# Optimization experiments

Measured on AMD Instinct MI355X. Metric: run time of the kernel, lower is better.

Reference implementation:

```python
import jax, jax.numpy as jnp
import numpy as np

DIM = 2048            # model dim
HID = 4096            # ssm inner dim (multiple_of*round(2/3*6144))
H = 64                # n_heads
P = HID // H          # head_dim = 64
N = 128               # state_dim
G = 1                 # n_groups
K = 4                 # conv_size
Q = 128               # chunk_size
CONV_DIM = HID + 2 * G * N       # 4352
D_IN = 2 * HID + 2 * G * N + H   # 8512
EPS = 1e-5


def _causal_conv_silu(xBC, w):
    # xBC: [B,L,C], w: [C,K]; depthwise causal conv1d fused with SiLU
    kern = w.T[:, None, :]  # [K,1,C]
    y = jax.lax.conv_general_dilated(
        xBC, kern, window_strides=(1,), padding=[(K - 1, 0)],
        dimension_numbers=('NHC', 'HIO', 'NHC'),
        feature_group_count=xBC.shape[-1])
    return y * jax.nn.sigmoid(y)


def _ssm(x, W_in, conv_w, dt_bias, A_log, D, norm_w, W_out):
    Bsz, L, _ = x.shape
    zxbcdt = x @ W_in.T                       # [B,L,D_IN]
    z = zxbcdt[..., :HID]                     # gate
    xBC = zxbcdt[..., HID:HID + CONV_DIM]
    dt_raw = zxbcdt[..., HID + CONV_DIM:]     # [B,L,H]

    xBC = _causal_conv_silu(xBC, conv_w)
    xs = xBC[..., :HID].reshape(Bsz, L, H, P)
    rep = H // G
    Bh = jnp.repeat(xBC[..., HID:HID + G * N].reshape(Bsz, L, G, N), rep, axis=2)  # [B,L,H,N]
    Ch = jnp.repeat(xBC[..., HID + G * N:].reshape(Bsz, L, G, N), rep, axis=2)

    dt = jax.nn.softplus(dt_raw + dt_bias)    # [B,L,H], dt_softplus=True
    A = -jnp.exp(A_log)                       # [H]

    # ---- chunked selective scan (Mamba2 SSD), chunk size Q ----
    nc = L // Q
    a = (dt * A).reshape(Bsz, nc, Q, H)
    cum = jnp.cumsum(a, axis=2)               # inclusive within-chunk cumsum, <= 0
    xs_c = xs.reshape(Bsz, nc, Q, H, P)
    dtc = dt.reshape(Bsz, nc, Q, H)
    Bc = Bh.reshape(Bsz, nc, Q, H, N)
    Cc = Ch.reshape(Bsz, nc, Q, H, N)

    # intra-chunk (diagonal) part: Y[i] += sum_{j<=i} exp(cum_i-cum_j) dt_j (C_i.B_j) x_j
    diff = cum[:, :, :, None, :] - cum[:, :, None, :, :]     # [b,c,i,j,h]
    tril = jnp.tril(jnp.ones((Q, Q), bool))[None, None, :, :, None]
    Lmat = jnp.exp(jnp.where(tril, diff, -jnp.inf))          # causal decay matrix
    CB = jnp.einsum('bcihn,bcjhn->bcijh', Cc, Bc)
    M = CB * Lmat * dtc[:, :, None, :, :]
    Yd = jnp.einsum('bcijh,bcjhp->bcihp', M, xs_c)

    # per-chunk end state: sum_j exp(cum_last-cum_j) dt_j x_j (x) B_j
    wdec = jnp.exp(cum[:, :, -1:, :] - cum) * dtc            # [b,c,q,h]
    states = jnp.einsum('bcqh,bcqhn,bcqhp->bchpn', wdec, Bc, xs_c)
    chunk_decay = jnp.exp(cum[:, :, -1, :])                  # [b,c,h]

    # inter-chunk recurrence over nc chunks
    def step(S, inp):
        dec, st = inp                                        # [b,h], [b,h,p,n]
        return S * dec[..., None, None] + st, S              # emit state entering chunk
    S0 = jnp.zeros((Bsz, H, P, N), x.dtype)
    _, Sprev = jax.lax.scan(step, S0,
                            (chunk_decay.transpose(1, 0, 2),
                             states.transpose(1, 0, 2, 3, 4)))
    Sprev = Sprev.transpose(1, 0, 2, 3, 4)                   # [b,c,h,p,n]

    # inter-chunk (off-diagonal) contribution
    Yoff = jnp.einsum('bcqh,bcqhn,bchpn->bcqhp', jnp.exp(cum), Cc, Sprev)

    y = (Yd + Yoff).reshape(Bsz, L, H, P) + D[None, None, :, None] * xs  # skip D
    y = y.reshape(Bsz, L, HID)

    yz = y * (z * jax.nn.sigmoid(z))                         # gated: y * silu(z)
    yn = yz * jax.lax.rsqrt(jnp.mean(yz * yz, axis=-1, keepdims=True) + EPS) * norm_w
    return yn @ W_out.T


def setup_inputs() -> dict:
    key = jax.random.key(0)
    k = jax.random.split(key, 6)
    return {
        'x': jax.random.normal(k[0], (2, 4096, DIM), jnp.float32),
        'W_in': jax.random.normal(k[1], (D_IN, DIM), jnp.float32) * DIM ** -0.5,
        'conv_w': jax.random.normal(k[2], (CONV_DIM, K), jnp.float32) * K ** -0.5,
        'dt_bias': jax.random.uniform(k[3], (H,), jnp.float32, minval=0.001, maxval=0.1),
        'A_log': jnp.log(jax.random.uniform(k[4], (H,), jnp.float32, minval=1.0, maxval=16.0)),
        'D': jnp.ones((H,), jnp.float32),
        'norm_w': jnp.ones((HID,), jnp.float32),
        'W_out': jax.random.normal(k[5], (DIM, HID), jnp.float32) * HID ** -0.5,
    }


def reference(x, W_in, conv_w, dt_bias, A_log, D, norm_w, W_out):
    return _ssm(x, W_in, conv_w, dt_bias, A_log, D, norm_w, W_out)
```

## Files before the change

### kernel.cpp

```cpp
#include <hip/hip_runtime.h>
#include <hip/hip_fp16.h>
#include <math.h>

#define ROWS   8192
#define DIMK   2048
#define HIDN   4096
#define QCH    128
#define NCHUNK 32

typedef __attribute__((ext_vector_type(8))) short short8;
typedef __attribute__((ext_vector_type(8))) _Float16 half8;
typedef __attribute__((ext_vector_type(4))) float floatx4;

static __device__ inline unsigned short f2h(float f){
  union { _Float16 h; unsigned short u; } v; v.h = (_Float16)f; return v.u;
}
static __device__ inline float h2f(unsigned short u){
  union { unsigned short u; _Float16 h; } v; v.u = u; return (float)v.h;
}
static __device__ inline void async_cp16(const void* g, void* l){
  __builtin_amdgcn_global_load_lds((const __attribute__((address_space(1))) void*)g,
                                   (__attribute__((address_space(3))) void*)l, 16, 0, 0);
}

__global__ void k_cast(const float* __restrict__ in, unsigned short* __restrict__ out, int n4){
  int i = blockIdx.x * 256 + threadIdx.x;
  if (i < n4){
    float4 v = ((const float4*)in)[i];
    unsigned long long p = (unsigned long long)f2h(v.x)
                         | ((unsigned long long)f2h(v.y) << 16)
                         | ((unsigned long long)f2h(v.z) << 32)
                         | ((unsigned long long)f2h(v.w) << 48);
    ((unsigned long long*)out)[i] = p;
  }
}

__global__ __launch_bounds__(256)
void k_dtraw(const float* __restrict__ x, const float* __restrict__ Win,
             float* __restrict__ dtraw){
  __shared__ float ws[64 * 132];
  const int t = threadIdx.x;
  const int lane = t & 63, w = t >> 6;
  const int r0 = blockIdx.x * 16;
  const int rw = __builtin_amdgcn_readfirstlane(r0 + w * 4);
  float a0 = 0.f, a1 = 0.f, a2 = 0.f, a3 = 0.f;
  for (int k0 = 0; k0 < DIMK; k0 += 128){
    __syncthreads();
#pragma unroll
    for (int l = 0; l < 8; l++){
      int fidx = (l * 256 + t) * 4;
      int row = fidx >> 7, col = fidx & 127;
      *(float4*)&ws[row * 132 + col] =
          *(const float4*)&Win[(size_t)(8448 + row) * DIMK + k0 + col];
    }
    __syncthreads();
    const float* xp = x + (size_t)rw * DIMK + k0;
#pragma unroll 8
    for (int kk = 0; kk < 128; kk += 4){
      float4 wv = *(const float4*)&ws[lane * 132 + kk];
      float4 v0 = *(const float4*)&xp[kk];
      float4 v1 = *(const float4*)&xp[DIMK + kk];
      float4 v2 = *(const float4*)&xp[2*DIMK + kk];
      float4 v3 = *(const float4*)&xp[3*DIMK + kk];
      a0 += wv.x*v0.x + wv.y*v0.y + wv.z*v0.z + wv.w*v0.w;
      a1 += wv.x*v1.x + wv.y*v1.y + wv.z*v1.z + wv.w*v1.w;
      a2 += wv.x*v2.x + wv.y*v2.y + wv.z*v2.z + wv.w*v2.w;
      a3 += wv.x*v3.x + wv.y*v3.y + wv.z*v3.z + wv.w*v3.w;
    }
  }
  dtraw[(size_t)rw * 64 + lane]       = a0;
  dtraw[((size_t)rw + 1) * 64 + lane] = a1;
  dtraw[((size_t)rw + 2) * 64 + lane] = a2;
  dtraw[((size_t)rw + 3) * 64 + lane] = a3;
}

template<int KD>
__device__ inline void gemm256_core(const unsigned short* __restrict__ A,
                                    const unsigned short* __restrict__ B,
                                    int row0, int col0,
                                    unsigned short* sA, unsigned short* sB,
                                    floatx4 (&acc)[8][4], int t){
  const int lane = t & 63, wid = t >> 6;
  const int wm = wid >> 2, wn = wid & 3;
  const int quad = lane >> 4, l16 = lane & 15;
  const int srow  = t >> 3;
  const int sslot = (t & 7) ^ (srow & 7);
  constexpr int NT = KD / 64;

  auto stageA = [&](int d, int half, int kt){
    unsigned short* dst = sA + d*256*64 + half*128*64;
    const unsigned short* src = A + (size_t)(row0 + half*128) * KD + kt*64;
#pragma unroll
    for (int i = 0; i < 2; i++)
      async_cp16(src + (size_t)(i*64 + srow) * KD + sslot*8,
                 dst + ((size_t)i*512 + t)*8);
  };
  auto stageB = [&](int d, int half, int kt){
    unsigned short* dst = sB + d*256*64 + half*128*64;
    const unsigned short* src = B + (size_t)(col0 + half*128) * KD + kt*64;
#pragma unroll
    for (int i = 0; i < 2; i++)
      async_cp16(src + (size_t)(i*64 + srow) * KD + sslot*8,
                 dst + ((size_t)i*512 + t)*8);
  };

  half8 af[4][2], bf[2][2];
  auto loadA = [&](const unsigned short* cA, int h){
#pragma unroll
    for (int mm = 0; mm < 4; mm++)
#pragma unroll
      for (int ks = 0; ks < 2; ks++)
        af[mm][ks] = *(const half8*)&cA[((h*4+mm)*16 + l16)*64 + (((ks*4+quad)^(l16&7))*8)];
  };
  auto loadB = [&](const unsigned short* cB, int h){
#pragma unroll
    for (int nn = 0; nn < 2; nn++)
#pragma unroll
      for (int ks = 0; ks < 2; ks++)
        bf[nn][ks] = *(const half8*)&cB[((h*2+nn)*16 + l16)*64 + (((ks*4+quad)^(l16&7))*8)];
  };
  auto mmac = [&](int mh, int nh){
    __builtin_amdgcn_s_setprio(1);
#pragma unroll
    for (int mm = 0; mm < 4; mm++)
#pragma unroll
      for (int nn = 0; nn < 2; nn++)
#pragma unroll
        for (int ks = 0; ks < 2; ks++)
          acc[mh*4+mm][nh*2+nn] = __builtin_amdgcn_mfma_f32_16x16x32_f16(
              af[mm][ks], bf[nn][ks], acc[mh*4+mm][nh*2+nn], 0, 0, 0);
    __builtin_amdgcn_s_setprio(0);
  };

  stageA(0,0,0); stageA(0,1,0); stageB(0,0,0); stageB(0,1,0);
  stageA(1,0,1); stageA(1,1,1);
  asm volatile("s_waitcnt vmcnt(4)" ::: "memory");
  __builtin_amdgcn_s_barrier();

  for (int T = 0; T < NT; T++){
    const int cur = T & 1;
    const unsigned short* cA = sA + cur*256*64 + wm*128*64;
    const unsigned short* cB = sB + cur*256*64 + wn*64*64;
    loadA(cA, 0); loadB(cB, 0);
    if (T + 1 < NT) stageB(cur^1, 0, T+1);
    __builtin_amdgcn_s_barrier();
    mmac(0, 0);
    __builtin_amdgcn_s_barrier();
    loadB(cB, 1);
    if (T + 1 < NT) stageB(cur^1, 1, T+1);
    __builtin_amdgcn_s_barrier();
    mmac(0, 1);
    __builtin_amdgcn_s_barrier();
    loadA(cA, 1);
    if (T + 2 < NT) stageA(cur, 0, T+2);
    __builtin_amdgcn_s_barrier();
    mmac(1, 1);
    __builtin_amdgcn_s_barrier();
    loadB(cB, 0);
    if (T + 2 < NT) stageA(cur, 1, T+2);
    if (T + 2 < NT)      { asm volatile("s_waitcnt vmcnt(4)" ::: "memory"); }
    else if (T + 1 < NT) { asm volatile("s_waitcnt vmcnt(0)" ::: "memory"); }
    __builtin_amdgcn_s_barrier();
    mmac(1, 0);
    __builtin_amdgcn_s_barrier();
  }
}

__global__ __launch_bounds__(512, 2)
void k_gemm1(const unsigned short* __restrict__ A, const unsigned short* __restrict__ B,
             unsigned short* __restrict__ zbuf, unsigned short* __restrict__ xsraw,
             unsigned short* __restrict__ bcraw){
  __shared__ __align__(16) unsigned short sA[2*256*64];
  __shared__ __align__(16) unsigned short sB[2*256*64];
  const int t = threadIdx.x;
  int swz = (blockIdx.x % 8) * 132 + blockIdx.x / 8;
  const int row0 = (swz & 31) * 256, col0 = (swz >> 5) * 256;
  floatx4 acc[8][4] = {};
  gemm256_core<DIMK>(A, B, row0, col0, sA, sB, acc, t);
  const int lane = t & 63, wid = t >> 6;
  const int wm = wid >> 2, wn = wid & 3;
  const int quad = lane >> 4, l16 = lane & 15;
  unsigned short* dst; int cbase, ldd;
  if (col0 < 4096){ dst = zbuf; cbase = 0; ldd = 4096; }
  else if (col0 < 8192){ dst = xsraw; cbase = 4096; ldd = 4096; }
  else { dst = bcraw; cbase = 8192; ldd = 256; }
#pragma unroll
  for (int m = 0; m < 8; m++)
#pragma unroll
    for (int n = 0; n < 4; n++){
      int rb = row0 + wm*128 + m*16 + quad*4;
      int cc = col0 + wn*64 + n*16 + l16 - cbase;
#pragma unroll
      for (int r = 0; r < 4; r++)
        dst[(size_t)(rb + r) * ldd + cc] = f2h(acc[m][n][r]);
    }
}

__global__ __launch_bounds__(512, 2)
void k_gemm2(const unsigned short* __restrict__ A, const unsigned short* __restrict__ B,
             float* __restrict__ C){
  __shared__ __align__(16) unsigned short sA[2*256*64];
  __shared__ __align__(16) unsigned short sB[2*256*64];
  const int t = threadIdx.x;
  int swz = (blockIdx.x % 8) * 32 + blockIdx.x / 8;
  const int row0 = (swz & 31) * 256, col0 = (swz >> 5) * 256;
  floatx4 acc[8][4] = {};
  gemm256_core<HIDN>(A, B, row0, col0, sA, sB, acc, t);
  const int lane = t & 63, wid = t >> 6;
  const int wm = wid >> 2, wn = wid & 3;
  const int quad = lane >> 4, l16 = lane & 15;
#pragma unroll
  for (int m = 0; m < 8; m++)
#pragma unroll
    for (int n = 0; n < 4; n++){
      int rb = row0 + wm*128 + m*16 + quad*4;
      int cc = col0 + wn*64 + n*16 + l16;
#pragma unroll
      for (int r = 0; r < 4; r++)
        C[(size_t)(rb + r) * DIMK + cc] = acc[m][n][r];
    }
}

__global__ void k_halo(const unsigned short* __restrict__ xsraw, unsigned short* __restrict__ halo){
  int col = blockIdx.x * 256 + threadIdx.x;
  int slot = blockIdx.y, bc = blockIdx.z;
  long r = (long)bc * QCH - 3 + slot;
  if (r >= 0)
    halo[((size_t)bc * 3 + slot) * 4096 + col] = xsraw[(size_t)r * 4096 + col];
}

__global__ void k_convbc(const unsigned short* __restrict__ bcraw, const float* __restrict__ cw,
                         unsigned short* __restrict__ bcc){
  int row = blockIdx.x, c = threadIdx.x;
  int tl = row & 4095;
  const float4 wv = *(const float4*)&cw[(size_t)(4096 + c) * 4];
  const unsigned short* col = bcraw + c;
  size_t rb = (size_t)row * 256;
  float a = h2f(col[rb]) * wv.w;
  if (tl >= 1) a += h2f(col[rb - 256]) * wv.z;
  if (tl >= 2) a += h2f(col[rb - 512]) * wv.y;
  if (tl >= 3) a += h2f(col[rb - 768]) * wv.x;
  bcc[rb + c] = f2h(a / (1.f + __expf(-a)));
}

__global__ void k_dtcum(const float* __restrict__ dtraw, const float* __restrict__ dtbias,
                        const float* __restrict__ Alog, float* __restrict__ dtb,
                        float* __restrict__ cumb){
  int bc = blockIdx.x;
  int h  = threadIdx.x;
  float bias = dtbias[h];
  float A = -__expf(Alog[h]);
  float run = 0.f;
  size_t rowb = (size_t)bc * QCH;
  for (int q = 0; q < QCH; q++){
    float dr = dtraw[(rowb + q) * 64 + h] + bias;
    float dt = dr > 20.f ? dr : log1pf(__expf(dr));
    dtb[(rowb + q) * 64 + h] = dt;
    run += dt * A;
    cumb[(rowb + q) * 64 + h] = run;
  }
}

__device__ inline void stage_xsT(const unsigned short* __restrict__ xsraw,
                                 const unsigned short* __restrict__ halo,
                                 const float* cws, unsigned short* xsT,
                                 int bc, int h, int t){
  const size_t rowb = (size_t)bc * QCH;
  const int tl0 = (bc & 31) * QCH;
#pragma unroll
  for (int it = 0; it < 2; it++){
    int idx = it * 256 + t;
    int q = idx & 127, p0 = (idx >> 7) * 16;
    int tl = tl0 + q;
    const unsigned short* cur = xsraw + (rowb + q) * 4096 + h * 64 + p0;
    const unsigned short* hb  = halo + ((size_t)bc * 3) * 4096 + h * 64 + p0;
    const unsigned short* r1 = (q >= 1) ? cur - 4096     : hb + 2 * 4096;
    const unsigned short* r2 = (q >= 2) ? cur - 2 * 4096 : hb + (size_t)(q + 1) * 4096;
    const unsigned short* r3 = (q >= 3) ? cur - 3 * 4096 : hb + (size_t)q * 4096;
    float f1 = (tl >= 1) ? 1.f : 0.f;
    float f2 = (tl >= 2) ? 1.f : 0.f;
    float f3 = (tl >= 3) ? 1.f : 0.f;
    short8 c0 = *(const short8*)cur, c1 = *(const short8*)(cur + 8);
    short8 a0 = *(const short8*)r1,  a1 = *(const short8*)(r1 + 8);
    short8 b0 = *(const short8*)r2,  b1 = *(const short8*)(r2 + 8);
    short8 d0 = *(const short8*)r3,  d1 = *(const short8*)(r3 + 8);
#pragma unroll
    for (int j = 0; j < 16; j++){
      int col = p0 + j;
      const float* wp = cws + col * 4;
      float vc = h2f((unsigned short)(j < 8 ? c0[j] : c1[j-8]));
      float v1 = h2f((unsigned short)(j < 8 ? a0[j] : a1[j-8]));
      float v2 = h2f((unsigned short)(j < 8 ? b0[j] : b1[j-8]));
      float v3 = h2f((unsigned short)(j < 8 ? d0[j] : d1[j-8]));
      float a = vc * wp[3] + f1 * v1 * wp[2] + f2 * v2 * wp[1] + f3 * v3 * wp[0];
      float s = a / (1.f + __expf(-a));
      xsT[col * 128 + q] = f2h(s);
    }
  }
}

__global__ __launch_bounds__(256, 2)
void k_chunk1(const unsigned short* __restrict__ xsc, const unsigned short* __restrict__ bcc,
              const float* __restrict__ dtb, const float* __restrict__ cumb,
              const float* __restrict__ Dp, const unsigned short* __restrict__ st,
              unsigned short* __restrict__ ybuf){
  __shared__ __align__(16) unsigned short Ml[128*128];
  __shared__ __align__(16) unsigned short xsT[64*128];
  __shared__ float cum_s[128], dt_s[128];
  const int blk = blockIdx.x, h = blk & 63, bc = blk >> 6;
  const size_t rowb = (size_t)bc * QCH;
  const int t = threadIdx.x, w = t >> 6, lane = t & 63, quad = lane >> 4, l16 = lane & 15;
  const int wrow = w * 32;
  if (t < 128){ cum_s[t] = cumb[(rowb + t)*64 + h]; dt_s[t] = dtb[(rowb + t)*64 + h]; }
  __syncthreads();
#pragma unroll
  for (int it = 0; it < 2; it++){
    int idx = it * 256 + t;
    int q = idx & 127, p0 = (idx >> 7) * 16;
    const unsigned short* cur = xsc + (rowb + q) * 4096 + h * 64 + p0;
    short8 c0 = *(const short8*)cur, c1 = *(const short8*)(cur + 8);
#pragma unroll
    for (int j = 0; j < 16; j++)
      xsT[(p0 + j) * 128 + q] = (unsigned short)(j < 8 ? c0[j] : c1[j-8]);
  }
  floatx4 acc[2][8] = {};
  const unsigned short* Cb = bcc + rowb * 256 + 128;
  const unsigned short* Bb = bcc + rowb * 256;
#pragma unroll
  for (int ks = 0; ks < 4; ks++){
    half8 af[2];
#pragma unroll
    for (int i = 0; i < 2; i++)
      af[i] = *(const half8*)(Cb + (size_t)(wrow + i*16 + l16) * 256 + ks*32 + quad*8);
#pragma unroll
    for (int j = 0; j < 8; j++){
      half8 bfr = *(const half8*)(Bb + (size_t)(j*16 + l16) * 256 + ks*32 + quad*8);
#pragma unroll
      for (int i = 0; i < 2; i++)
        acc[i][j] = __builtin_amdgcn_mfma_f32_16x16x32_f16(af[i], bfr, acc[i][j], 0, 0, 0);
    }
  }
#pragma unroll
  for (int i = 0; i < 2; i++)
#pragma unroll
    for (int j = 0; j < 8; j++){
      int jc = j*16 + l16;
      float dtj = dt_s[jc], cj = cum_s[jc];
#pragma unroll
      for (int r = 0; r < 4; r++){
        int ir = wrow + i*16 + quad*4 + r;
        float m = (ir >= jc) ? acc[i][j][r] * __expf(cum_s[ir] - cj) * dtj : 0.f;
        Ml[ir * 128 + jc] = f2h(m);
      }
    }
  __syncthreads();
  floatx4 accY[2][4] = {};
#pragma unroll
  for (int ks = 0; ks < 4; ks++){
    half8 af[2], bfr[4];
#pragma unroll
    for (int i = 0; i < 2; i++)
      af[i] = *(const half8*)&Ml[(wrow + i*16 + l16)*128 + ks*32 + quad*8];
#pragma unroll
    for (int p = 0; p < 4; p++)
      bfr[p] = *(const half8*)&xsT[(p*16 + l16)*128 + ks*32 + quad*8];
#pragma unroll
    for (int i = 0; i < 2; i++)
#pragma unroll
      for (int p = 0; p < 4; p++)
        accY[i][p] = __builtin_amdgcn_mfma_f32_16x16x32_f16(af[i], bfr[p], accY[i][p], 0, 0, 0);
  }
  __syncthreads();
  unsigned short* Sp = Ml;
  {
    size_t base = ((size_t)bc * 64 + h) * 8192;
#pragma unroll
    for (int it = 0; it < 4; it++){
      int idx = (it * 256 + t) * 8;
      *(short8*)&Sp[idx] = *(const short8*)&st[base + idx];
    }
  }
  __syncthreads();
  floatx4 accO[2][4] = {};
#pragma unroll
  for (int ks = 0; ks < 4; ks++){
    half8 af[2], bfr[4];
#pragma unroll
    for (int i = 0; i < 2; i++)
      af[i] = *(const half8*)(Cb + (size_t)(wrow + i*16 + l16) * 256 + ks*32 + quad*8);
#pragma unroll
    for (int p = 0; p < 4; p++)
      bfr[p] = *(const half8*)&Sp[(p*16 + l16)*128 + ks*32 + quad*8];
#pragma unroll
    for (int i = 0; i < 2; i++)
#pragma unroll
      for (int p = 0; p < 4; p++)
        accO[i][p] = __builtin_amdgcn_mfma_f32_16x16x32_f16(af[i], bfr[p], accO[i][p], 0, 0, 0);
  }
  float Dh = Dp[h];
#pragma unroll
  for (int i = 0; i < 2; i++)
#pragma unroll
    for (int p = 0; p < 4; p++){
      int pc = p*16 + l16;
#pragma unroll
      for (int r = 0; r < 4; r++){
        int ir = wrow + i*16 + quad*4 + r;
        float y = accY[i][p][r] + __expf(cum_s[ir]) * accO[i][p][r] + Dh * h2f(xsT[pc*128 + ir]);
        ybuf[(rowb + ir) * (size_t)HIDN + h*64 + pc] = f2h(y);
      }
    }
}

__global__ __launch_bounds__(256, 2)
void k_chunk2(unsigned short* __restrict__ xsraw, const unsigned short* __restrict__ bcc,
              const unsigned short* __restrict__ halo, const float* __restrict__ cw,
              const float* __restrict__ dtb, const float* __restrict__ cumb,
              unsigned short* __restrict__ st){
  __shared__ __align__(16) unsigned short wBT[128*128];
  __shared__ __align__(16) unsigned short xsT[64*128];
  __shared__ float cum_s[128], dt_s[128];
  __shared__ float cws[64*4];
  const int blk = blockIdx.x, h = blk & 63, bc = blk >> 6;
  const size_t rowb = (size_t)bc * QCH;
  const int t = threadIdx.x, w = t >> 6, lane = t & 63, quad = lane >> 4, l16 = lane & 15;
  if (t < 128){ cum_s[t] = cumb[(rowb + t)*64 + h]; dt_s[t] = dtb[(rowb + t)*64 + h]; }
  if (t < 64) *(float4*)&cws[t*4] = *(const float4*)&cw[((size_t)h*64 + t)*4];
  __syncthreads();
  stage_xsT(xsraw, halo, cws, xsT, bc, h, t);
  __syncthreads();
#pragma unroll
  for (int it = 0; it < 2; it++){
    int idx = it * 256 + t;
    int q = idx & 127, p0 = (idx >> 7) * 16;
    short8 w0, w1;
#pragma unroll
    for (int j = 0; j < 8; j++){
      w0[j] = (short)xsT[(p0 + j) * 128 + q];
      w1[j] = (short)xsT[(p0 + 8 + j) * 128 + q];
    }
    unsigned short* g = xsraw + (rowb + q) * 4096 + h * 64 + p0;
    *(short8*)g = w0;
    *(short8*)(g + 8) = w1;
  }
  float clast = cum_s[127];
#pragma unroll
  for (int it = 0; it < 2; it++){
    int idx = it * 256 + t;
    int q = idx & 127, n0 = (idx >> 7) * 32;
    float wd = __expf(clast - cum_s[q]) * dt_s[q];
    const unsigned short* gp = bcc + (rowb + q) * 256 + n0;
#pragma unroll
    for (int c4 = 0; c4 < 4; c4++){
      short8 v = *(const short8*)(gp + c4*8);
#pragma unroll
      for (int jj = 0; jj < 8; jj++)
        wBT[(n0 + c4*8 + jj)*128 + q] = f2h(h2f((unsigned short)v[jj]) * wd);
    }
  }
  __syncthreads();
  floatx4 acc[8] = {};
#pragma unroll
  for (int ks = 0; ks < 4; ks++){
    half8 af = *(const half8*)&xsT[(w*16 + l16)*128 + ks*32 + quad*8];
#pragma unroll
    for (int j = 0; j < 8; j++){
      half8 bfr = *(const half8*)&wBT[(j*16 + l16)*128 + ks*32 + quad*8];
      acc[j] = __builtin_amdgcn_mfma_f32_16x16x32_f16(af, bfr, acc[j], 0, 0, 0);
    }
  }
  size_t base = ((size_t)bc * 64 + h) * 8192;
#pragma unroll
  for (int j = 0; j < 8; j++){
    int n = j*16 + l16;
#pragma unroll
    for (int r = 0; r < 4; r++){
      int p = w*16 + quad*4 + r;
      st[base + p*128 + n] = f2h(acc[j][r]);
    }
  }
}

__global__ void k_scan(unsigned short* __restrict__ st, const float* __restrict__ cumb){
  int id = blockIdx.x * 256 + threadIdx.x;
  int n = id & 127, p = (id >> 7) & 63, h = (id >> 13) & 63, b = id >> 19;
  float S = 0.f;
  for (int c = 0; c < NCHUNK; c++){
    int bc = b * NCHUNK + c;
    size_t idx = ((size_t)bc * 64 + h) * 8192 + (size_t)p * 128 + n;
    float dec = __expf(cumb[((size_t)bc * QCH + 127) * 64 + h]);
    float v = h2f(st[idx]);
    st[idx] = f2h(S);
    S = S * dec + v;
  }
}

__global__ __launch_bounds__(256)
void k_gate(unsigned short* __restrict__ yb, const unsigned short* __restrict__ zb,
            const float* __restrict__ nw){
  __shared__ float red[4];
  int row = blockIdx.x, t = threadIdx.x;
  float vals[16], ss = 0.f;
#pragma unroll
  for (int it = 0; it < 16; it++){
    int c = it * 256 + t;
    float y = h2f(yb[(size_t)row * HIDN + c]);
    float z = h2f(zb[(size_t)row * HIDN + c]);
    float v = y * (z / (1.f + __expf(-z)));
    vals[it] = v; ss += v * v;
  }
  for (int o = 32; o > 0; o >>= 1) ss += __shfl_down(ss, o, 64);
  int w = t >> 6, lane = t & 63;
  if (lane == 0) red[w] = ss;
  __syncthreads();
  float scale = rsqrtf((red[0] + red[1] + red[2] + red[3]) / (float)HIDN + 1e-5f);
#pragma unroll
  for (int it = 0; it < 16; it++){
    int c = it * 256 + t;
    yb[(size_t)row * HIDN + c] = f2h(vals[it] * scale * nw[c]);
  }
}

extern "C" void kernel_launch(void* const* d_in, const int* in_sizes, int n_in,
                              void* d_out, int out_size, void* d_ws, size_t ws_size,
                              hipStream_t stream){
  const float* x      = (const float*)d_in[0];
  const float* Win    = (const float*)d_in[1];
  const float* convw  = (const float*)d_in[2];
  const float* dtbias = (const float*)d_in[3];
  const float* Alog   = (const float*)d_in[4];
  const float* Dp     = (const float*)d_in[5];
  const float* nw     = (const float*)d_in[6];
  const float* Wout   = (const float*)d_in[7];
  float* out = (float*)d_out;

  char* ws = (char*)d_ws;
  size_t off = 0;
  auto alloc = [&](size_t bytes)->void*{ void* p = ws + off; off += (bytes + 255) & ~(size_t)255; return p; };
  unsigned short* xw    = (unsigned short*)alloc((size_t)ROWS * DIMK * 2);
  unsigned short* winb  = (unsigned short*)alloc((size_t)8448 * DIMK * 2);
  float*          dtraw = (float*)alloc((size_t)ROWS * 64 * 4);
  unsigned short* woutb = (unsigned short*)alloc((size_t)DIMK * HIDN * 2);
  unsigned short* zbuf  = (unsigned short*)alloc((size_t)ROWS * HIDN * 2);
  unsigned short* xsraw = (unsigned short*)alloc((size_t)ROWS * HIDN * 2);
  unsigned short* bcraw = (unsigned short*)alloc((size_t)ROWS * 256 * 2);
  unsigned short* bcc   = (unsigned short*)alloc((size_t)ROWS * 256 * 2);
  unsigned short* halo  = (unsigned short*)alloc((size_t)64 * 3 * 4096 * 2);
  float*          dtb   = (float*)alloc((size_t)ROWS * 64 * 4);
  float*          cumb  = (float*)alloc((size_t)ROWS * 64 * 4);
  unsigned short* st    = xw;
  unsigned short* ybuf  = xsraw;

  k_cast<<<(ROWS*DIMK/4 + 255)/256, 256, 0, stream>>>(x, xw, ROWS*DIMK/4);
  k_cast<<<(8448*DIMK/4 + 255)/256, 256, 0, stream>>>(Win, winb, 8448*DIMK/4);
  k_cast<<<(DIMK*HIDN/4 + 255)/256, 256, 0, stream>>>(Wout, woutb, DIMK*HIDN/4);
  k_dtraw<<<ROWS/16, 256, 0, stream>>>(x, Win, dtraw);
  k_gemm1<<<dim3(33*32), 512, 0, stream>>>(xw, winb, zbuf, xsraw, bcraw);
  k_halo<<<dim3(16, 3, 64), 256, 0, stream>>>(xsraw, halo);
  k_convbc<<<ROWS, 256, 0, stream>>>(bcraw, convw, bcc);
  k_dtcum<<<64, 64, 0, stream>>>(dtraw, dtbias, Alog, dtb, cumb);
  k_chunk2<<<4096, 256, 0, stream>>>(xsraw, bcc, halo, convw, dtb, cumb, st);
  k_scan<<<4096, 256, 0, stream>>>(st, cumb);
  k_chunk1<<<4096, 256, 0, stream>>>(xsraw, bcc, dtb, cumb, Dp, st, ybuf);
  k_gate<<<ROWS, 256, 0, stream>>>(ybuf, zbuf, nw);
  k_gemm2<<<dim3(8*32), 512, 0, stream>>>(ybuf, woutb, out);
}
```

Baseline: 1.197 ms.

## Hold full A/B fragment sets in registers with inline-asm LDS reads in GEMM core

The GEMM main loop now keeps all eight A fragments and four B fragments of the K-tile in registers instead of reloading halves. It issues explicit ds_read_b128 instructions behind sched_barrier and lgkmcnt waits, and reorders the MFMA quadrants so each fragment is read from LDS only once per tile. This cuts LDS read traffic and removes one barrier phase, and both A-tile prefetches now go out together. The cost is more VGPRs under launch_bounds(512,2), which risks spills, and the hard lgkmcnt(0) waits block the compiler from interleaving reads with MFMAs.

```diff
diff --git a/kernel.cpp b/kernel.cpp
--- a/kernel.cpp
+++ b/kernel.cpp
@@ -74,6 +74,18 @@
   dtraw[((size_t)rw + 3) * 64 + lane] = a3;
 }
 
+static __device__ inline unsigned ldsaddr(const void* p){
+  return (unsigned)(size_t)(const __attribute__((address_space(3))) void*)p;
+}
+static __device__ inline floatx4 dsr128(unsigned a){
+  floatx4 d;
+  asm volatile("ds_read_b128 %0, %1" : "=v"(d) : "v"(a));
+  return d;
+}
+static __device__ inline half8 as_h8(floatx4 f){
+  union { floatx4 f; half8 h; } u; u.f = f; return u.h;
+}
+
 template<int KD>
 __device__ inline void gemm256_core(const unsigned short* __restrict__ A,
                                     const unsigned short* __restrict__ B,
@@ -104,20 +116,13 @@
                  dst + ((size_t)i*512 + t)*8);
   };
 
-  half8 af[4][2], bf[2][2];
-  auto loadA = [&](const unsigned short* cA, int h){
-#pragma unroll
-    for (int mm = 0; mm < 4; mm++)
-#pragma unroll
-      for (int ks = 0; ks < 2; ks++)
-        af[mm][ks] = *(const half8*)&cA[((h*4+mm)*16 + l16)*64 + (((ks*4+quad)^(l16&7))*8)];
+  const unsigned sAbase = ldsaddr(sA), sBbase = ldsaddr(sB);
+  floatx4 af[8][2], bf[4][2];
+  auto rdA = [&](unsigned base, int fr, int ks) -> floatx4 {
+    return dsr128(base + 2u*(unsigned)((fr*16 + l16)*64 + (((ks*4+quad)^(l16&7))*8)));
   };
-  auto loadB = [&](const unsigned short* cB, int h){
-#pragma unroll
-    for (int nn = 0; nn < 2; nn++)
-#pragma unroll
-      for (int ks = 0; ks < 2; ks++)
-        bf[nn][ks] = *(const half8*)&cB[((h*2+nn)*16 + l16)*64 + (((ks*4+quad)^(l16&7))*8)];
+  auto rdB = [&](unsigned base, int fc, int ks) -> floatx4 {
+    return dsr128(base + 2u*(unsigned)((fc*16 + l16)*64 + (((ks*4+quad)^(l16&7))*8)));
   };
   auto mmac = [&](int mh, int nh){
     __builtin_amdgcn_s_setprio(1);
@@ -128,7 +133,7 @@
 #pragma unroll
         for (int ks = 0; ks < 2; ks++)
           acc[mh*4+mm][nh*2+nn] = __builtin_amdgcn_mfma_f32_16x16x32_f16(
-              af[mm][ks], bf[nn][ks], acc[mh*4+mm][nh*2+nn], 0, 0, 0);
+              as_h8(af[mh*4+mm][ks]), as_h8(bf[nh*2+nn][ks]), acc[mh*4+mm][nh*2+nn], 0, 0, 0);
     __builtin_amdgcn_s_setprio(0);
   };
 
@@ -139,29 +144,53 @@
 
   for (int T = 0; T < NT; T++){
     const int cur = T & 1;
-    const unsigned short* cA = sA + cur*256*64 + wm*128*64;
-    const unsigned short* cB = sB + cur*256*64 + wn*64*64;
-    loadA(cA, 0); loadB(cB, 0);
+    const unsigned aAd = sAbase + 2u*(unsigned)(cur*256*64 + wm*128*64);
+    const unsigned bAd = sBbase + 2u*(unsigned)(cur*256*64 + wn*64*64);
+#pragma unroll
+    for (int fr = 0; fr < 4; fr++)
+#pragma unroll
+      for (int ks = 0; ks < 2; ks++)
+        af[fr][ks] = rdA(aAd, fr, ks);
+#pragma unroll
+    for (int fc = 0; fc < 2; fc++)
+#pragma unroll
+      for (int ks = 0; ks < 2; ks++)
+        bf[fc][ks] = rdB(bAd, fc, ks);
     if (T + 1 < NT) stageB(cur^1, 0, T+1);
     __builtin_amdgcn_s_barrier();
+    asm volatile("s_waitcnt lgkmcnt(0)" ::: "memory");
+    __builtin_amdgcn_sched_barrier(0);
     mmac(0, 0);
     __builtin_amdgcn_s_barrier();
-    loadB(cB, 1);
+#pragma unroll
+    for (int fr = 4; fr < 8; fr++)
+#pragma unroll
+      for (int ks = 0; ks < 2; ks++)
+        af[fr][ks] = rdA(aAd, fr, ks);
     if (T + 1 < NT) stageB(cur^1, 1, T+1);
     __builtin_amdgcn_s_barrier();
+    asm volatile("s_waitcnt lgkmcnt(0)" ::: "memory");
+    __builtin_amdgcn_sched_barrier(0);
+    mmac(1, 0);
+    __builtin_amdgcn_s_barrier();
+#pragma unroll
+    for (int fc = 2; fc < 4; fc++)
+#pragma unroll
+      for (int ks = 0; ks < 2; ks++)
+        bf[fc][ks] = rdB(bAd, fc, ks);
+    __builtin_amdgcn_s_barrier();
+    asm volatile("s_waitcnt lgkmcnt(0)" ::: "memory");
+    __builtin_amdgcn_sched_barrier(0);
     mmac(0, 1);
     __builtin_amdgcn_s_barrier();
-    loadA(cA, 1);
-    if (T + 2 < NT) stageA(cur, 0, T+2);
+    if (T + 2 < NT){
+      stageA(cur, 0, T+2); stageA(cur, 1, T+2);
+      asm volatile("s_waitcnt vmcnt(4)" ::: "memory");
+    } else if (T + 1 < NT){
+      asm volatile("s_waitcnt vmcnt(0)" ::: "memory");
+    }
     __builtin_amdgcn_s_barrier();
     mmac(1, 1);
-    __builtin_amdgcn_s_barrier();
-    loadB(cB, 0);
-    if (T + 2 < NT) stageA(cur, 1, T+2);
-    if (T + 2 < NT)      { asm volatile("s_waitcnt vmcnt(4)" ::: "memory"); }
-    else if (T + 1 < NT) { asm volatile("s_waitcnt vmcnt(0)" ::: "memory"); }
-    __builtin_amdgcn_s_barrier();
-    mmac(1, 0);
     __builtin_amdgcn_s_barrier();
   }
 }
```

Result: faster. 1.092 ms (-8.8%).
